# Performance work log

Measured on AMD Instinct MI355X. Metric: run time of the kernel, lower is better.

Reference implementation:

```python
import jax, jax.numpy as jnp
import numpy as np

N_NODES = 50000
N_EDGES = 800000
D_IN = 512
LATENT = [512, 512, 512]
L2_EPS = 1e-12  # torch F.normalize clamp_min


def _gin_layer(x, src, dst, W, b, eps):
    # sum aggregation of neighbor (source) features into destination nodes
    agg = jax.ops.segment_sum(x[src], dst, num_segments=x.shape[0])  # [N, d]
    h = agg + (1.0 + eps) * x
    return jax.nn.relu(h @ W + b)  # Sequential(Linear, ReLU)


def _l2_normalize(x):
    n = jnp.sqrt(jnp.sum(x * x, axis=-1, keepdims=True))
    return x / jnp.maximum(n, L2_EPS)


def setup_inputs() -> dict:
    key = jax.random.key(0)
    ks = jax.random.split(key, 10)
    x = jax.random.normal(ks[0], (N_NODES, D_IN), dtype=jnp.float32)
    edge_index = jax.random.randint(ks[1], (2, N_EDGES), 0, N_NODES, dtype=jnp.int32)
    dims = [D_IN] + LATENT
    inp = {"x": x, "edge_index": edge_index}
    for i in range(3):
        fan_in = dims[i]
        bound = 1.0 / np.sqrt(fan_in)
        inp[f"W{i+1}"] = jax.random.uniform(ks[2 + 2 * i], (dims[i], dims[i + 1]), jnp.float32, -bound, bound)
        inp[f"b{i+1}"] = jax.random.uniform(ks[3 + 2 * i], (dims[i + 1],), jnp.float32, -bound, bound)
        inp[f"eps{i+1}"] = jnp.zeros((), dtype=jnp.float32)  # train_eps=True, init 0
    return inp


def reference(x, edge_index, W1, b1, eps1, W2, b2, eps2, W3, b3, eps3):
    src, dst = edge_index[0], edge_index[1]
    # layers 0..num_layers-2: GINConv -> L2 normalize -> ReLU
    h = _gin_layer(x, src, dst, W1, b1, eps1)
    h = jax.nn.relu(_l2_normalize(h))
    h = _gin_layer(h, src, dst, W2, b2, eps2)
    h = jax.nn.relu(_l2_normalize(h))
    # final layer: raw GINConv output = logits
    logits = _gin_layer(h, src, dst, W3, b3, eps3)
    probs = jax.nn.softmax(logits, axis=-1)
    return (logits, probs)
```

## Files before the change

### kernel.cpp

```cpp
#include <hip/hip_runtime.h>
#include <stdint.h>

#define N_NODES 50000
#define N_EDGES 800000

typedef unsigned int uint32;

__device__ inline float bflo(uint32 u) { return __builtin_bit_cast(float, u << 16); }
__device__ inline float bfhi(uint32 u) { return __builtin_bit_cast(float, u & 0xffff0000u); }
__device__ inline float bf2f(unsigned short h) { return __builtin_bit_cast(float, (uint32)h << 16); }
__device__ inline unsigned short f2bf(float f) {
    uint32 u = __builtin_bit_cast(uint32, f);
    u += 0x7fffu + ((u >> 16) & 1u);
    return (unsigned short)(u >> 16);
}
__device__ inline uint32 pack2(float lo, float hi) {
    return (uint32)f2bf(lo) | ((uint32)f2bf(hi) << 16);
}

__global__ __launch_bounds__(256) void zero_k(int* p, int n) {
    int i = blockIdx.x * 256 + threadIdx.x;
    if (i < n) p[i] = 0;
}

__global__ __launch_bounds__(256) void count_k(const int* __restrict__ ei, int* __restrict__ cnt) {
    int e = blockIdx.x * 256 + threadIdx.x;
    if (e < N_EDGES) atomicAdd(&cnt[ei[N_EDGES + e]], 1);
}

#define NB 196

__global__ __launch_bounds__(256) void blocksum_k(const int* __restrict__ cnt, int* __restrict__ bsum) {
    int i = blockIdx.x * 256 + threadIdx.x;
    int v = (i < N_NODES) ? cnt[i] : 0;
#pragma unroll
    for (int off = 32; off > 0; off >>= 1) v += __shfl_down(v, off);
    __shared__ int sh[4];
    int w = threadIdx.x >> 6, lane = threadIdx.x & 63;
    if (lane == 0) sh[w] = v;
    __syncthreads();
    if (threadIdx.x == 0) bsum[blockIdx.x] = sh[0] + sh[1] + sh[2] + sh[3];
}

__global__ __launch_bounds__(256) void bscan_k(const int* __restrict__ bsum, int* __restrict__ bpre,
                                               int* __restrict__ rowptr) {
    __shared__ int sh[256];
    int t = threadIdx.x;
    int v = (t < NB) ? bsum[t] : 0;
    sh[t] = v;
    __syncthreads();
    for (int d = 1; d < 256; d <<= 1) {
        int u = (t >= d) ? sh[t - d] : 0;
        __syncthreads();
        sh[t] += u;
        __syncthreads();
    }
    if (t < NB) bpre[t] = sh[t] - v;
    if (t == NB - 1) rowptr[N_NODES] = sh[t];
}

__global__ __launch_bounds__(256) void scatter_k(int* __restrict__ cnt, const int* __restrict__ bpre,
                                                 int* __restrict__ rowptr) {
    int b = blockIdx.x, t = threadIdx.x, i = b * 256 + t;
    int w = t >> 6, lane = t & 63;
    int myv = (i < N_NODES) ? cnt[i] : 0;
    int v = myv;
#pragma unroll
    for (int d = 1; d < 64; d <<= 1) {
        int u = __shfl_up(v, d);
        if (lane >= d) v += u;
    }
    __shared__ int wt[4];
    if (lane == 63) wt[w] = v;
    __syncthreads();
    int off = bpre[b];
    for (int k = 0; k < w; k++) off += wt[k];
    int excl = v - myv + off;
    if (i < N_NODES) {
        rowptr[i] = excl;
        cnt[i] = excl;
    }
}

__global__ __launch_bounds__(256) void fill_k(const int* __restrict__ ei, int* __restrict__ cursor,
                                              int* __restrict__ csr) {
    int e = blockIdx.x * 256 + threadIdx.x;
    if (e < N_EDGES) {
        int d = ei[N_EDGES + e];
        int p = atomicAdd(&cursor[d], 1);
        csr[p] = ei[e];
    }
}

__global__ __launch_bounds__(256) void wprep_k(const float* __restrict__ W,
                                               unsigned short* __restrict__ Whi,
                                               unsigned short* __restrict__ Wlo) {
    __shared__ float sh[64][65];
    int bk = (blockIdx.x & 7) * 64;
    int bn = (blockIdx.x >> 3) * 64;
    int t = threadIdx.x;
    int lr = t >> 4;
    int lc4 = (t & 15) * 4;
#pragma unroll
    for (int i = 0; i < 4; i++) {
        int k = lr + i * 16;
        float4 v = *(const float4*)&W[(size_t)(bk + k) * 512 + bn + lc4];
        sh[k][lc4] = v.x; sh[k][lc4 + 1] = v.y; sh[k][lc4 + 2] = v.z; sh[k][lc4 + 3] = v.w;
    }
    __syncthreads();
#pragma unroll
    for (int i = 0; i < 4; i++) {
        int n = lr + i * 16;
        float w0 = sh[lc4][n], w1 = sh[lc4 + 1][n], w2 = sh[lc4 + 2][n], w3 = sh[lc4 + 3][n];
        ushort4 h, l;
        h.x = f2bf(w0); l.x = f2bf(w0 - bf2f(h.x));
        h.y = f2bf(w1); l.y = f2bf(w1 - bf2f(h.y));
        h.z = f2bf(w2); l.z = f2bf(w2 - bf2f(h.z));
        h.w = f2bf(w3); l.w = f2bf(w3 - bf2f(h.w));
        *(ushort4*)&Whi[(size_t)(bn + n) * 512 + bk + lc4] = h;
        *(ushort4*)&Wlo[(size_t)(bn + n) * 512 + bk + lc4] = l;
    }
}

__global__ __launch_bounds__(256) void xconv_k(const float4* __restrict__ x, uint2* __restrict__ xb) {
    int i = blockIdx.x * 256 + threadIdx.x;
    float4 v = x[i];
    uint2 o;
    o.x = pack2(v.x, v.y);
    o.y = pack2(v.z, v.w);
    xb[i] = o;
}

__global__ __launch_bounds__(256) void invn_k(const float* __restrict__ ss, float* __restrict__ invn) {
    int i = blockIdx.x * 256 + threadIdx.x;
    if (i < N_NODES) invn[i] = 1.0f / fmaxf(sqrtf(ss[i]), 1e-12f);
}

#define ACCW(Q, W)                                                            \
    a0 = fmaf(W, bflo(Q.x), a0); a1 = fmaf(W, bfhi(Q.x), a1);                 \
    a2 = fmaf(W, bflo(Q.y), a2); a3 = fmaf(W, bfhi(Q.y), a3);                 \
    a4 = fmaf(W, bflo(Q.z), a4); a5 = fmaf(W, bfhi(Q.z), a5);                 \
    a6 = fmaf(W, bflo(Q.w), a6); a7 = fmaf(W, bfhi(Q.w), a7);

template <bool SCALED>
__global__ __launch_bounds__(256) void agg_k(const uint4* __restrict__ xin,
                                             const int* __restrict__ rowptr,
                                             const int* __restrict__ csr,
                                             const float* __restrict__ eps,
                                             const float* __restrict__ invn,
                                             uint4* __restrict__ hout) {
    int node = blockIdx.x * 4 + (threadIdx.x >> 6);
    int lane = threadIdx.x & 63;
    int beg = rowptr[node], end = rowptr[node + 1];
    float a0 = 0.f, a1 = 0.f, a2 = 0.f, a3 = 0.f, a4 = 0.f, a5 = 0.f, a6 = 0.f, a7 = 0.f;
    int e = beg;
    for (; e + 8 <= end; e += 8) {
        int s0 = csr[e],     s1 = csr[e + 1], s2 = csr[e + 2], s3 = csr[e + 3];
        int s4 = csr[e + 4], s5 = csr[e + 5], s6 = csr[e + 6], s7 = csr[e + 7];
        uint4 q0 = xin[(size_t)s0 * 64 + lane];
        uint4 q1 = xin[(size_t)s1 * 64 + lane];
        uint4 q2 = xin[(size_t)s2 * 64 + lane];
        uint4 q3 = xin[(size_t)s3 * 64 + lane];
        uint4 q4 = xin[(size_t)s4 * 64 + lane];
        uint4 q5 = xin[(size_t)s5 * 64 + lane];
        uint4 q6 = xin[(size_t)s6 * 64 + lane];
        uint4 q7 = xin[(size_t)s7 * 64 + lane];
        float w0 = SCALED ? invn[s0] : 1.0f;
        float w1 = SCALED ? invn[s1] : 1.0f;
        float w2 = SCALED ? invn[s2] : 1.0f;
        float w3 = SCALED ? invn[s3] : 1.0f;
        float w4 = SCALED ? invn[s4] : 1.0f;
        float w5 = SCALED ? invn[s5] : 1.0f;
        float w6 = SCALED ? invn[s6] : 1.0f;
        float w7 = SCALED ? invn[s7] : 1.0f;
        ACCW(q0, w0) ACCW(q1, w1) ACCW(q2, w2) ACCW(q3, w3)
        ACCW(q4, w4) ACCW(q5, w5) ACCW(q6, w6) ACCW(q7, w7)
    }
    for (; e < end; ++e) {
        int s0 = csr[e];
        uint4 q0 = xin[(size_t)s0 * 64 + lane];
        float w0 = SCALED ? invn[s0] : 1.0f;
        ACCW(q0, w0)
    }
    uint4 qs = xin[(size_t)node * 64 + lane];
    float wsf = (1.0f + eps[0]) * (SCALED ? invn[node] : 1.0f);
    ACCW(qs, wsf)
    uint4 o;
    o.x = pack2(a0, a1);
    o.y = pack2(a2, a3);
    o.z = pack2(a4, a5);
    o.w = pack2(a6, a7);
    hout[(size_t)node * 64 + lane] = o;
}

typedef __bf16 bf16x8 __attribute__((ext_vector_type(8)));
typedef float f32x4 __attribute__((ext_vector_type(4)));

__device__ inline void async16(const void* g, void* l) {
    __builtin_amdgcn_global_load_lds((const __attribute__((address_space(1))) void*)g,
                                     (__attribute__((address_space(3))) void*)l, 16, 0, 0);
}

template <bool SPLIT, bool F32OUT, bool NORM>
__global__ __launch_bounds__(256) void gemm_k(const unsigned short* __restrict__ A,
                                              const unsigned short* __restrict__ Whi,
                                              const unsigned short* __restrict__ Wlo,
                                              const float* __restrict__ bias,
                                              unsigned short* __restrict__ outB,
                                              float* __restrict__ outF,
                                              float* __restrict__ ssOut, int M) {
    constexpr int K = 512, N = 512, BK = 32, TM = 128, NK = K / BK;
    constexpr int BUF = TM * BK;
    __shared__ unsigned short lds_a[2 * BUF];
    __shared__ unsigned short lds_bh[2 * BUF];
    __shared__ unsigned short lds_bl[SPLIT ? 2 * BUF : 16];
    const int t = threadIdx.x;
    const int w = t >> 6, lane = t & 63;
    const int wrow = w >> 1, wcol = w & 1;

    const int nwg = gridDim.x;
    const int qd = nwg >> 3, rd = nwg & 7;
    const int xcd = blockIdx.x & 7, jj = blockIdx.x >> 3;
    const int wg = (xcd < rd ? xcd * (qd + 1) : rd * (qd + 1) + (xcd - rd) * qd) + jj;
    const int m0 = (wg >> 2) * TM;
    const int n0 = (wg & 3) * TM;

    int r0 = w * 16 + (lane >> 2), cc = (lane & 3) * 8;
    int r1 = 64 + r0;
    int am0 = m0 + r0; am0 = am0 < M ? am0 : M - 1;
    int am1 = m0 + r1; am1 = am1 < M ? am1 : M - 1;
    const unsigned short* ag0 = A + (size_t)am0 * K + cc;
    const unsigned short* ag1 = A + (size_t)am1 * K + cc;
    const unsigned short* bh0 = Whi + (size_t)(n0 + r0) * K + cc;
    const unsigned short* bh1 = Whi + (size_t)(n0 + r1) * K + cc;
    const unsigned short* bl0 = Wlo + (size_t)(n0 + r0) * K + cc;
    const unsigned short* bl1 = Wlo + (size_t)(n0 + r1) * K + cc;
    const int wo = w * 512;

    f32x4 acc[4][4] = {};
    const int quad = lane >> 4, l15 = lane & 15;
    const int arow = wrow * 64 + l15;
    const int brow = wcol * 64 + l15;

    auto stage = [&](int k0, int buf) {
        unsigned short* da = lds_a + buf * BUF + wo;
        unsigned short* dh = lds_bh + buf * BUF + wo;
        async16(ag0 + k0, da);
        async16(ag1 + k0, da + 2048);
        async16(bh0 + k0, dh);
        async16(bh1 + k0, dh + 2048);
        if (SPLIT) {
            unsigned short* dl = lds_bl + buf * BUF + wo;
            async16(bl0 + k0, dl);
            async16(bl1 + k0, dl + 2048);
        }
    };

    auto compute = [&](int buf) {
        const unsigned short* ba = lds_a + buf * BUF;
        const unsigned short* bb = lds_bh + buf * BUF;
        bf16x8 af[4], bhf[4], blf[4];
#pragma unroll
        for (int i = 0; i < 4; i++)
            af[i] = *(const bf16x8*)&ba[(arow + i * 16) * BK + quad * 8];
#pragma unroll
        for (int j = 0; j < 4; j++)
            bhf[j] = *(const bf16x8*)&bb[(brow + j * 16) * BK + quad * 8];
        if (SPLIT) {
            const unsigned short* bl = lds_bl + buf * BUF;
#pragma unroll
            for (int j = 0; j < 4; j++)
                blf[j] = *(const bf16x8*)&bl[(brow + j * 16) * BK + quad * 8];
        }
#pragma unroll
        for (int i = 0; i < 4; i++)
#pragma unroll
            for (int j = 0; j < 4; j++) {
                acc[i][j] = __builtin_amdgcn_mfma_f32_16x16x32_bf16(af[i], bhf[j], acc[i][j], 0, 0, 0);
                if (SPLIT)
                    acc[i][j] = __builtin_amdgcn_mfma_f32_16x16x32_bf16(af[i], blf[j], acc[i][j], 0, 0, 0);
            }
    };

    stage(0, 0);
    __syncthreads();
    int cur = 0;
    for (int ks = 0; ks < NK - 1; ++ks) {
        stage((ks + 1) * BK, cur ^ 1);
        compute(cur);
        __syncthreads();
        cur ^= 1;
    }
    compute(cur);

#pragma unroll
    for (int i = 0; i < 4; i++) {
        int mbase = m0 + wrow * 64 + i * 16 + quad * 4;
        float rs[4] = {0.f, 0.f, 0.f, 0.f};
#pragma unroll
        for (int j = 0; j < 4; j++) {
            int n = n0 + wcol * 64 + j * 16 + l15;
            float bv = bias[n];
#pragma unroll
            for (int r = 0; r < 4; r++) {
                int m = mbase + r;
                if (m < M) {
                    float v = fmaxf(acc[i][j][r] + bv, 0.0f);
                    if (NORM) rs[r] += v * v;
                    if (F32OUT) outF[(size_t)m * N + n] = v;
                    else        outB[(size_t)m * N + n] = f2bf(v);
                }
            }
        }
        if (NORM) {
#pragma unroll
            for (int r = 0; r < 4; r++) {
                float s = rs[r];
                s += __shfl_xor(s, 1);
                s += __shfl_xor(s, 2);
                s += __shfl_xor(s, 4);
                s += __shfl_xor(s, 8);
                int m = mbase + r;
                if (l15 == 0 && m < M) atomicAdd(&ssOut[m], s);
            }
        }
    }
}

__global__ __launch_bounds__(256) void softmax_k(const float* __restrict__ logits,
                                                 float* __restrict__ probs) {
    int node = blockIdx.x * 4 + (threadIdx.x >> 6);
    int lane = threadIdx.x & 63;
    const float4* zp = (const float4*)(logits + (size_t)node * 512);
    float4 q0 = zp[lane * 2], q1 = zp[lane * 2 + 1];
    float f[8] = {q0.x, q0.y, q0.z, q0.w, q1.x, q1.y, q1.z, q1.w};
    float m = f[0];
#pragma unroll
    for (int i = 1; i < 8; i++) m = fmaxf(m, f[i]);
#pragma unroll
    for (int off = 32; off > 0; off >>= 1) m = fmaxf(m, __shfl_xor(m, off));
    float e[8], s = 0.f;
#pragma unroll
    for (int i = 0; i < 8; i++) { e[i] = __expf(f[i] - m); s += e[i]; }
#pragma unroll
    for (int off = 32; off > 0; off >>= 1) s += __shfl_xor(s, off);
    float inv = 1.0f / s;
    float4* pp = (float4*)(probs + (size_t)node * 512);
    pp[lane * 2]     = make_float4(e[0] * inv, e[1] * inv, e[2] * inv, e[3] * inv);
    pp[lane * 2 + 1] = make_float4(e[4] * inv, e[5] * inv, e[6] * inv, e[7] * inv);
}

extern "C" void kernel_launch(void* const* d_in, const int* in_sizes, int n_in,
                              void* d_out, int out_size, void* d_ws, size_t ws_size,
                              hipStream_t stream) {
    (void)in_sizes; (void)n_in; (void)out_size; (void)ws_size;
    const float* x = (const float*)d_in[0];
    const int* ei = (const int*)d_in[1];
    const float* W1 = (const float*)d_in[2];
    const float* b1 = (const float*)d_in[3];
    const float* e1 = (const float*)d_in[4];
    const float* W2 = (const float*)d_in[5];
    const float* b2 = (const float*)d_in[6];
    const float* e2 = (const float*)d_in[7];
    const float* W3 = (const float*)d_in[8];
    const float* b3 = (const float*)d_in[9];
    const float* e3 = (const float*)d_in[10];
    float* out = (float*)d_out;
    float* out_logits = out;
    float* out_probs = out + (size_t)N_NODES * 512;

    char* ws = (char*)d_ws;
    int* rowptr = (int*)ws;
    int* cursor = rowptr + 50048;
    int* csr = cursor + 50048;
    int* bsum = csr + N_EDGES;
    int* bpre = bsum + 256;
    float* invn = (float*)(bpre + 256);
    float* ss = invn + 50048;
    float* ss1 = ss;
    float* ss2 = ss + 50048;
    unsigned short* Wsp = (unsigned short*)(ss + 2 * 50048);
    unsigned short* f0 = Wsp + 3 * 524288;
    unsigned short* fA = f0 + (size_t)N_NODES * 512;
    unsigned short* f1 = fA + (size_t)N_NODES * 512;

    zero_k<<<196, 256, 0, stream>>>(cursor, N_NODES);
    zero_k<<<392, 256, 0, stream>>>((int*)ss, 2 * 50048);
    count_k<<<(N_EDGES + 255) / 256, 256, 0, stream>>>(ei, cursor);
    blocksum_k<<<NB, 256, 0, stream>>>(cursor, bsum);
    bscan_k<<<1, 256, 0, stream>>>(bsum, bpre, rowptr);
    scatter_k<<<NB, 256, 0, stream>>>(cursor, bpre, rowptr);
    fill_k<<<(N_EDGES + 255) / 256, 256, 0, stream>>>(ei, cursor, csr);

    wprep_k<<<64, 256, 0, stream>>>(W1, Wsp,           Wsp + 262144);
    wprep_k<<<64, 256, 0, stream>>>(W2, Wsp + 524288,  Wsp + 786432);
    wprep_k<<<64, 256, 0, stream>>>(W3, Wsp + 1048576, Wsp + 1310720);

    xconv_k<<<25000, 256, 0, stream>>>((const float4*)x, (uint2*)f0);

    const int GG = 4 * ((N_NODES + 127) / 128);

    agg_k<false><<<12500, 256, 0, stream>>>((const uint4*)f0, rowptr, csr, e1, nullptr, (uint4*)fA);
    gemm_k<false, false, true><<<GG, 256, 0, stream>>>(fA, Wsp, Wsp + 262144, b1, f1, nullptr, ss1, N_NODES);
    invn_k<<<196, 256, 0, stream>>>(ss1, invn);
    agg_k<true><<<12500, 256, 0, stream>>>((const uint4*)f1, rowptr, csr, e2, invn, (uint4*)fA);
    gemm_k<false, false, true><<<GG, 256, 0, stream>>>(fA, Wsp + 524288, Wsp + 786432, b2, f1, nullptr, ss2, N_NODES);
    invn_k<<<196, 256, 0, stream>>>(ss2, invn);
    agg_k<true><<<12500, 256, 0, stream>>>((const uint4*)f1, rowptr, csr, e3, invn, (uint4*)fA);
    gemm_k<true, true, false><<<GG, 256, 0, stream>>>(fA, Wsp + 1048576, Wsp + 1310720, b3, nullptr, out_logits, nullptr, N_NODES);
    softmax_k<<<N_NODES / 4, 256, 0, stream>>>(out_logits, out_probs);
}
```

Baseline: 989.5 us.

## Reorder GEMM before aggregation and fuse bias/ReLU/L2-normalize into aggregation

For the first two layers, the linear transform is applied before neighbor aggregation, using linearity of the sum. Bias, ReLU and L2 normalization move into the aggregation kernel's epilogue via a wavefront reduction. This removes the per-node sum-of-squares atomics, the invn kernels, the zeroing kernel and per-edge norm-scale gathers. It changes where bf16 rounding happens (on XW rather than on the aggregated sum), which may shift numerical error slightly.

```diff
diff --git a/kernel.cpp b/kernel.cpp
--- a/kernel.cpp
+++ b/kernel.cpp
@@ -131,23 +131,16 @@
     xb[i] = o;
 }
 
-__global__ __launch_bounds__(256) void invn_k(const float* __restrict__ ss, float* __restrict__ invn) {
-    int i = blockIdx.x * 256 + threadIdx.x;
-    if (i < N_NODES) invn[i] = 1.0f / fmaxf(sqrtf(ss[i]), 1e-12f);
-}
-
-#define ACCW(Q, W)                                                            \
-    a0 = fmaf(W, bflo(Q.x), a0); a1 = fmaf(W, bfhi(Q.x), a1);                 \
-    a2 = fmaf(W, bflo(Q.y), a2); a3 = fmaf(W, bfhi(Q.y), a3);                 \
-    a4 = fmaf(W, bflo(Q.z), a4); a5 = fmaf(W, bfhi(Q.z), a5);                 \
-    a6 = fmaf(W, bflo(Q.w), a6); a7 = fmaf(W, bfhi(Q.w), a7);
-
-template <bool SCALED>
+#define ACC8(Q)                                                          \
+    a0 += bflo(Q.x); a1 += bfhi(Q.x); a2 += bflo(Q.y); a3 += bfhi(Q.y);  \
+    a4 += bflo(Q.z); a5 += bfhi(Q.z); a6 += bflo(Q.w); a7 += bfhi(Q.w);
+
+template <bool NORM>
 __global__ __launch_bounds__(256) void agg_k(const uint4* __restrict__ xin,
                                              const int* __restrict__ rowptr,
                                              const int* __restrict__ csr,
                                              const float* __restrict__ eps,
-                                             const float* __restrict__ invn,
+                                             const float* __restrict__ bias,
                                              uint4* __restrict__ hout) {
     int node = blockIdx.x * 4 + (threadIdx.x >> 6);
     int lane = threadIdx.x & 63;
@@ -165,31 +158,43 @@
         uint4 q5 = xin[(size_t)s5 * 64 + lane];
         uint4 q6 = xin[(size_t)s6 * 64 + lane];
         uint4 q7 = xin[(size_t)s7 * 64 + lane];
-        float w0 = SCALED ? invn[s0] : 1.0f;
-        float w1 = SCALED ? invn[s1] : 1.0f;
-        float w2 = SCALED ? invn[s2] : 1.0f;
-        float w3 = SCALED ? invn[s3] : 1.0f;
-        float w4 = SCALED ? invn[s4] : 1.0f;
-        float w5 = SCALED ? invn[s5] : 1.0f;
-        float w6 = SCALED ? invn[s6] : 1.0f;
-        float w7 = SCALED ? invn[s7] : 1.0f;
-        ACCW(q0, w0) ACCW(q1, w1) ACCW(q2, w2) ACCW(q3, w3)
-        ACCW(q4, w4) ACCW(q5, w5) ACCW(q6, w6) ACCW(q7, w7)
+        ACC8(q0) ACC8(q1) ACC8(q2) ACC8(q3)
+        ACC8(q4) ACC8(q5) ACC8(q6) ACC8(q7)
     }
     for (; e < end; ++e) {
         int s0 = csr[e];
         uint4 q0 = xin[(size_t)s0 * 64 + lane];
-        float w0 = SCALED ? invn[s0] : 1.0f;
-        ACCW(q0, w0)
+        ACC8(q0)
     }
     uint4 qs = xin[(size_t)node * 64 + lane];
-    float wsf = (1.0f + eps[0]) * (SCALED ? invn[node] : 1.0f);
-    ACCW(qs, wsf)
+    float ws = 1.0f + eps[0];
+    a0 = fmaf(ws, bflo(qs.x), a0); a1 = fmaf(ws, bfhi(qs.x), a1);
+    a2 = fmaf(ws, bflo(qs.y), a2); a3 = fmaf(ws, bfhi(qs.y), a3);
+    a4 = fmaf(ws, bflo(qs.z), a4); a5 = fmaf(ws, bfhi(qs.z), a5);
+    a6 = fmaf(ws, bflo(qs.w), a6); a7 = fmaf(ws, bfhi(qs.w), a7);
+
     uint4 o;
-    o.x = pack2(a0, a1);
-    o.y = pack2(a2, a3);
-    o.z = pack2(a4, a5);
-    o.w = pack2(a6, a7);
+    if (NORM) {
+        float4 b0 = *(const float4*)(bias + lane * 8);
+        float4 b1 = *(const float4*)(bias + lane * 8 + 4);
+        float h0 = fmaxf(a0 + b0.x, 0.f), h1 = fmaxf(a1 + b0.y, 0.f);
+        float h2 = fmaxf(a2 + b0.z, 0.f), h3 = fmaxf(a3 + b0.w, 0.f);
+        float h4 = fmaxf(a4 + b1.x, 0.f), h5 = fmaxf(a5 + b1.y, 0.f);
+        float h6 = fmaxf(a6 + b1.z, 0.f), h7 = fmaxf(a7 + b1.w, 0.f);
+        float ssl = h0 * h0 + h1 * h1 + h2 * h2 + h3 * h3 + h4 * h4 + h5 * h5 + h6 * h6 + h7 * h7;
+#pragma unroll
+        for (int off = 32; off > 0; off >>= 1) ssl += __shfl_xor(ssl, off);
+        float inv = 1.0f / fmaxf(sqrtf(ssl), 1e-12f);
+        o.x = pack2(h0 * inv, h1 * inv);
+        o.y = pack2(h2 * inv, h3 * inv);
+        o.z = pack2(h4 * inv, h5 * inv);
+        o.w = pack2(h6 * inv, h7 * inv);
+    } else {
+        o.x = pack2(a0, a1);
+        o.y = pack2(a2, a3);
+        o.z = pack2(a4, a5);
+        o.w = pack2(a6, a7);
+    }
     hout[(size_t)node * 64 + lane] = o;
 }
 
@@ -201,14 +206,13 @@
                                      (__attribute__((address_space(3))) void*)l, 16, 0, 0);
 }
 
-template <bool SPLIT, bool F32OUT, bool NORM>
+template <bool SPLIT, bool F32OUT>
 __global__ __launch_bounds__(256) void gemm_k(const unsigned short* __restrict__ A,
                                               const unsigned short* __restrict__ Whi,
                                               const unsigned short* __restrict__ Wlo,
                                               const float* __restrict__ bias,
                                               unsigned short* __restrict__ outB,
-                                              float* __restrict__ outF,
-                                              float* __restrict__ ssOut, int M) {
+                                              float* __restrict__ outF, int M) {
     constexpr int K = 512, N = 512, BK = 32, TM = 128, NK = K / BK;
     constexpr int BUF = TM * BK;
     __shared__ unsigned short lds_a[2 * BUF];
@@ -296,32 +300,20 @@
 #pragma unroll
     for (int i = 0; i < 4; i++) {
         int mbase = m0 + wrow * 64 + i * 16 + quad * 4;
-        float rs[4] = {0.f, 0.f, 0.f, 0.f};
 #pragma unroll
         for (int j = 0; j < 4; j++) {
             int n = n0 + wcol * 64 + j * 16 + l15;
-            float bv = bias[n];
+            float bv = F32OUT ? bias[n] : 0.0f;
 #pragma unroll
             for (int r = 0; r < 4; r++) {
                 int m = mbase + r;
                 if (m < M) {
-                    float v = fmaxf(acc[i][j][r] + bv, 0.0f);
-                    if (NORM) rs[r] += v * v;
-                    if (F32OUT) outF[(size_t)m * N + n] = v;
-                    else        outB[(size_t)m * N + n] = f2bf(v);
+                    if (F32OUT) {
+                        outF[(size_t)m * N + n] = fmaxf(acc[i][j][r] + bv, 0.0f);
+                    } else {
+                        outB[(size_t)m * N + n] = f2bf(acc[i][j][r]);
+                    }
                 }
-            }
-        }
-        if (NORM) {
-#pragma unroll
-            for (int r = 0; r < 4; r++) {
-                float s = rs[r];
-                s += __shfl_xor(s, 1);
-                s += __shfl_xor(s, 2);
-                s += __shfl_xor(s, 4);
-                s += __shfl_xor(s, 8);
-                int m = mbase + r;
-                if (l15 == 0 && m < M) atomicAdd(&ssOut[m], s);
             }
         }
     }
@@ -375,17 +367,11 @@
     int* csr = cursor + 50048;
     int* bsum = csr + N_EDGES;
     int* bpre = bsum + 256;
-    float* invn = (float*)(bpre + 256);
-    float* ss = invn + 50048;
-    float* ss1 = ss;
-    float* ss2 = ss + 50048;
-    unsigned short* Wsp = (unsigned short*)(ss + 2 * 50048);
-    unsigned short* f0 = Wsp + 3 * 524288;
-    unsigned short* fA = f0 + (size_t)N_NODES * 512;
-    unsigned short* f1 = fA + (size_t)N_NODES * 512;
+    unsigned short* Wsp = (unsigned short*)(bpre + 256);
+    unsigned short* fa = Wsp + 3 * 524288;
+    unsigned short* fb = fa + (size_t)N_NODES * 512;
 
     zero_k<<<196, 256, 0, stream>>>(cursor, N_NODES);
-    zero_k<<<392, 256, 0, stream>>>((int*)ss, 2 * 50048);
     count_k<<<(N_EDGES + 255) / 256, 256, 0, stream>>>(ei, cursor);
     blocksum_k<<<NB, 256, 0, stream>>>(cursor, bsum);
     bscan_k<<<1, 256, 0, stream>>>(bsum, bpre, rowptr);
@@ -396,17 +382,15 @@
     wprep_k<<<64, 256, 0, stream>>>(W2, Wsp + 524288,  Wsp + 786432);
     wprep_k<<<64, 256, 0, stream>>>(W3, Wsp + 1048576, Wsp + 1310720);
 
-    xconv_k<<<25000, 256, 0, stream>>>((const float4*)x, (uint2*)f0);
+    xconv_k<<<25000, 256, 0, stream>>>((const float4*)x, (uint2*)fa);
 
     const int GG = 4 * ((N_NODES + 127) / 128);
 
-    agg_k<false><<<12500, 256, 0, stream>>>((const uint4*)f0, rowptr, csr, e1, nullptr, (uint4*)fA);
-    gemm_k<false, false, true><<<GG, 256, 0, stream>>>(fA, Wsp, Wsp + 262144, b1, f1, nullptr, ss1, N_NODES);
-    invn_k<<<196, 256, 0, stream>>>(ss1, invn);
-    agg_k<true><<<12500, 256, 0, stream>>>((const uint4*)f1, rowptr, csr, e2, invn, (uint4*)fA);
-    gemm_k<false, false, true><<<GG, 256, 0, stream>>>(fA, Wsp + 524288, Wsp + 786432, b2, f1, nullptr, ss2, N_NODES);
-    invn_k<<<196, 256, 0, stream>>>(ss2, invn);
-    agg_k<true><<<12500, 256, 0, stream>>>((const uint4*)f1, rowptr, csr, e3, invn, (uint4*)fA);
-    gemm_k<true, true, false><<<GG, 256, 0, stream>>>(fA, Wsp + 1048576, Wsp + 1310720, b3, nullptr, out_logits, nullptr, N_NODES);
+    gemm_k<false, false><<<GG, 256, 0, stream>>>(fa, Wsp, Wsp + 262144, nullptr, fb, nullptr, N_NODES);
+    agg_k<true><<<12500, 256, 0, stream>>>((const uint4*)fb, rowptr, csr, e1, b1, (uint4*)fa);
+    gemm_k<false, false><<<GG, 256, 0, stream>>>(fa, Wsp + 524288, Wsp + 786432, nullptr, fb, nullptr, N_NODES);
+    agg_k<true><<<12500, 256, 0, stream>>>((const uint4*)fb, rowptr, csr, e2, b2, (uint4*)fa);
+    agg_k<false><<<12500, 256, 0, stream>>>((const uint4*)fa, rowptr, csr, e3, nullptr, (uint4*)fb);
+    gemm_k<true, true><<<GG, 256, 0, stream>>>(fb, Wsp + 1048576, Wsp + 1310720, b3, nullptr, out_logits, N_NODES);
     softmax_k<<<N_NODES / 4, 256, 0, stream>>>(out_logits, out_probs);
 }
```

New measurement: 938.9 us. 1.05x faster.
